# Performance work log

Hardware: AMD Instinct MI355X
Metric: run time of the kernel (lower is better)

## Reference

```python
import jax, jax.numpy as jnp
import numpy as np

# DeTok Decoder ('base'): width=768, layers=12, heads=12, head_dim=64, grid=16, seq=256
B, N, G, P = 64, 256, 16, 16
W, L, H, D = 768, 12, 12, 64
HID, TC = 2048, 16  # SwiGLU hidden = int(2/3*768*4.0); token_channels
EPS = 1e-6


def make_rope(dim=D, seq_h=G, seq_w=G, max_freq=7.0, min_freq=0.0007):
    f1 = max_freq * (max_freq / min_freq) ** np.linspace(0, -1, dim // 4)
    f1 = np.concatenate([f1, f1])                      # [dim//2]
    f2 = np.zeros((2, dim))
    f2[0, : dim // 2] = f1
    f2[1, dim // 2 :] = f1
    f2 = f2 * 2.0 * np.pi
    cx = np.linspace(0, 1, seq_h)
    cy = np.linspace(0, 1, seq_w)
    coords = np.stack(np.meshgrid(cx, cy, indexing='ij'), -1).reshape(-1, 2)  # cartesian_prod order
    ang = coords @ f2                                   # [N, dim]
    return np.concatenate([np.cos(ang), np.sin(ang)], -1).astype(np.float32)  # [N, 2*dim]


def setup_inputs() -> dict:
    key = jax.random.key(0)
    ks = jax.random.split(key, 16)
    s = 0.02
    inp = {
        'z_latents': jax.random.normal(ks[0], (B, N, TC), jnp.float32),
        'pos_emb':   jax.random.normal(ks[1], (1, N, W), jnp.float32) * (W ** -0.5),
        'W_embed':   jax.random.normal(ks[2], (TC, W), jnp.float32) * s,
        'b_embed':   jnp.zeros((W,), jnp.float32),
        'ln_pre_w':  jnp.ones((W,), jnp.float32),
        'n1_w':      jnp.ones((L, W), jnp.float32),
        'qkv_w':     jax.random.normal(ks[3], (L, W, 3 * W), jnp.float32) * s,
        'qkv_b':     jnp.zeros((L, 3 * W), jnp.float32),
        'proj_w':    jax.random.normal(ks[4], (L, W, W), jnp.float32) * s,
        'proj_b':    jnp.zeros((L, W), jnp.float32),
        'n2_w':      jnp.ones((L, W), jnp.float32),
        'w12_w':     jax.random.normal(ks[5], (L, W, 2 * HID), jnp.float32) * s,
        'w12_b':     jnp.zeros((L, 2 * HID), jnp.float32),
        'w3_w':      jax.random.normal(ks[6], (L, HID, W), jnp.float32) * s,
        'w3_b':      jnp.zeros((L, W), jnp.float32),
        'ln_post_w': jnp.ones((W,), jnp.float32),
        'conv1_w':   jax.random.normal(ks[7], (W, P * P * 3), jnp.float32) * s,  # 1x1 conv as matmul
        'conv1_b':   jnp.zeros((P * P * 3,), jnp.float32),
        'conv_out_w': jax.random.normal(ks[8], (3, 3, 3, 3), jnp.float32) * s,   # OIHW
        'conv_out_b': jnp.zeros((3,), jnp.float32),
        'rope':      jnp.asarray(make_rope()),          # [N, 2*D] buffer
    }
    return inp


def _rms(x, w):
    return x * jax.lax.rsqrt(jnp.mean(x * x, axis=-1, keepdims=True) + EPS) * w


def _rotate_half(x):
    x1, x2 = x[..., 0::2], x[..., 1::2]
    return jnp.stack((-x2, x1), axis=-1).reshape(x.shape)


def reference(z_latents, pos_emb, W_embed, b_embed, ln_pre_w, n1_w, qkv_w, qkv_b,
              proj_w, proj_b, n2_w, w12_w, w12_b, w3_w, w3_b, ln_post_w,
              conv1_w, conv1_b, conv_out_w, conv_out_b, rope):
    bsz = z_latents.shape[0]
    cos = rope[None, None, :, :D]   # [1,1,N,D]
    sin = rope[None, None, :, D:]
    scale = 1.0 / jnp.sqrt(jnp.float32(D))

    z = z_latents @ W_embed + b_embed          # [B,N,W]
    z = z + pos_emb
    z = _rms(z, ln_pre_w)

    def block(z, p):
        n1, qw, qb, pw, pb, n2, a12w, a12b, a3w, a3b = p
        h = _rms(z, n1)
        qkv = (h @ qw + qb).reshape(bsz, N, 3, H, D).transpose(2, 0, 3, 1, 4)  # [3,B,H,N,D]
        q, k, v = qkv[0], qkv[1], qkv[2]
        q = q * cos + _rotate_half(q) * sin
        k = k * cos + _rotate_half(k) * sin
        att = jax.nn.softmax(jnp.einsum('bhnd,bhmd->bhnm', q, k) * scale, axis=-1)
        o = jnp.einsum('bhnm,bhmd->bhnd', att, v).transpose(0, 2, 1, 3).reshape(bsz, N, W)
        z = z + o @ pw + pb
        h = _rms(z, n2)
        x12 = h @ a12w + a12b
        x1, x2 = x12[..., :HID], x12[..., HID:]
        z = z + (jax.nn.silu(x1) * x2) @ a3w + a3b
        return z, None

    z, _ = jax.lax.scan(block, z, (n1_w, qkv_w, qkv_b, proj_w, proj_b,
                                   n2_w, w12_w, w12_b, w3_w, w3_b))
    z = _rms(z, ln_post_w)
    # 1x1 conv (width -> P*P*3) then pixel-unshuffle: b (h w) (p1 p2 c) -> b c (h p1) (w p2)
    y = z @ conv1_w + conv1_b                   # [B,N,P*P*3]
    y = y.reshape(bsz, G, G, P, P, 3).transpose(0, 5, 1, 3, 2, 4).reshape(bsz, 3, G * P, G * P)
    out = jax.lax.conv_general_dilated(y, conv_out_w, (1, 1), 'SAME',
                                       dimension_numbers=('NCHW', 'OIHW', 'NCHW'))
    return out + conv_out_b[None, :, None, None]
```

## Files before the change

kernel.cpp:

```cpp
#include <hip/hip_runtime.h>
#include <stdint.h>

typedef unsigned short u16;
typedef __attribute__((ext_vector_type(8))) short short8;
typedef __attribute__((ext_vector_type(4))) float f32x4;

__device__ __forceinline__ float bflo(unsigned int u) {
  union { unsigned int i; float f; } x; x.i = u << 16; return x.f;
}
__device__ __forceinline__ float bfhi(unsigned int u) {
  union { unsigned int i; float f; } x; x.i = u & 0xffff0000u; return x.f;
}
__device__ __forceinline__ float bf2f(u16 u) {
  union { unsigned int i; float f; } x; x.i = ((unsigned int)u) << 16; return x.f;
}
__device__ __forceinline__ u16 f2bf(float f) {
  union { float f; unsigned int i; } x; x.f = f;
  unsigned int r = x.i + 0x7fffu + ((x.i >> 16) & 1u);
  return (u16)(r >> 16);
}

typedef __attribute__((address_space(1))) const unsigned int as1_uint;
typedef __attribute__((address_space(3))) unsigned int as3_uint;

__device__ __forceinline__ void gload_lds16(const void* g, void* l) {
  __builtin_amdgcn_global_load_lds(
      (const as1_uint*)(unsigned long long)g,
      (as3_uint*)(unsigned int)(unsigned long long)l,
      16, 0, 0);
}

__device__ __forceinline__ short8 dsr128(const void* p) {
  short8 r;
  asm volatile("ds_read_b128 %0, %1"
               : "=v"(r)
               : "v"((unsigned int)(unsigned long long)p));
  return r;
}

#define FENCE() asm volatile("" ::: "memory")
#define BAR() do { FENCE(); __builtin_amdgcn_s_barrier(); FENCE(); } while (0)
#define VMCNT(n) asm volatile("s_waitcnt vmcnt(" #n ")" ::: "memory")
#define LGKM0_SB() do { asm volatile("s_waitcnt lgkmcnt(0)"); __builtin_amdgcn_sched_barrier(0); } while (0)

__global__ __launch_bounds__(256) void transpose_conv(const float* __restrict__ in, u16* __restrict__ out,
                                                      int K, int N, int perm) {
  __shared__ float tile[32][33];
  const long l = blockIdx.z;
  int nb = blockIdx.x;
  int nbsrc = nb;
  if (perm == 2) {
    nbsrc = (nb & 1) ? 64 + (nb >> 1) : (nb >> 1);
  }
  const int nbS = nbsrc * 32;
  const int nbD = nb * 32;
  const int kb = blockIdx.y * 32;
  const float* I = in + l * (long)K * N;
  u16* O = out + l * (long)N * K;
  const int tx = threadIdx.x, ty = threadIdx.y;
#pragma unroll
  for (int i = 0; i < 32; i += 8)
    tile[ty + i][tx] = I[(long)(kb + ty + i) * N + nbS + tx];
  __syncthreads();
#pragma unroll
  for (int i = 0; i < 32; i += 8)
    O[(long)(nbD + ty + i) * K + kb + tx] = f2bf(tile[tx][ty + i]);
}

__global__ __launch_bounds__(256) void embed_kernel(const float* __restrict__ zl, const float* __restrict__ pos,
                                                    const float* __restrict__ We, const float* __restrict__ be,
                                                    const float* __restrict__ lnw, float* __restrict__ z) {
  const long row = blockIdx.x;
  const int n = (int)(row & 255);
  const int t = threadIdx.x;
  __shared__ float zc[16];
  __shared__ float wsum[4];
  if (t < 16) zc[t] = zl[row * 16 + t];
  __syncthreads();
  float v[3];
#pragma unroll
  for (int e = 0; e < 3; ++e) {
    const int col = t + e * 256;
    float s = be[col] + pos[(long)n * 768 + col];
#pragma unroll
    for (int c = 0; c < 16; ++c) s += zc[c] * We[c * 768 + col];
    v[e] = s;
  }
  float ss = v[0] * v[0] + v[1] * v[1] + v[2] * v[2];
#pragma unroll
  for (int off = 32; off > 0; off >>= 1) ss += __shfl_down(ss, off, 64);
  if ((t & 63) == 0) wsum[t >> 6] = ss;
  __syncthreads();
  const float tot = wsum[0] + wsum[1] + wsum[2] + wsum[3];
  const float rs = rsqrtf(tot * (1.f / 768.f) + 1e-6f);
#pragma unroll
  for (int e = 0; e < 3; ++e) {
    const int col = t + e * 256;
    z[row * 768 + col] = v[e] * rs * lnw[col];
  }
}

__global__ __launch_bounds__(256) void rms_wave(const float* __restrict__ z, const float* __restrict__ w,
                                                u16* __restrict__ h) {
  const int lane = threadIdx.x & 63;
  const int wv = threadIdx.x >> 6;
  float4 wl[3];
#pragma unroll
  for (int k = 0; k < 3; ++k) wl[k] = *(const float4*)(w + k * 256 + lane * 4);
  const long base = ((long)blockIdx.x * 4 + wv) * 8;
  for (int r = 0; r < 8; ++r) {
    const long row = base + r;
    const float* zr = z + row * 768;
    float4 xv[3];
    float ss = 0.f;
#pragma unroll
    for (int k = 0; k < 3; ++k) {
      xv[k] = *(const float4*)(zr + k * 256 + lane * 4);
      ss += xv[k].x * xv[k].x + xv[k].y * xv[k].y + xv[k].z * xv[k].z + xv[k].w * xv[k].w;
    }
#pragma unroll
    for (int o = 1; o < 64; o <<= 1) ss += __shfl_xor(ss, o);
    const float rs = rsqrtf(ss * (1.f / 768.f) + 1e-6f);
    u16* hr = h + row * 768;
#pragma unroll
    for (int k = 0; k < 3; ++k) {
      uint2 pk;
      pk.x = (unsigned int)f2bf(xv[k].x * rs * wl[k].x) | ((unsigned int)f2bf(xv[k].y * rs * wl[k].y) << 16);
      pk.y = (unsigned int)f2bf(xv[k].z * rs * wl[k].z) | ((unsigned int)f2bf(xv[k].w * rs * wl[k].w) << 16);
      *(uint2*)(hr + k * 256 + lane * 4) = pk;
    }
  }
}

template <int OUT_MODE>
__global__ __launch_bounds__(256, 3) void gemm128s(const u16* __restrict__ A, const u16* __restrict__ Bt,
                                                   void* __restrict__ C, const float* __restrict__ bias,
                                                   int M, int N, int K, int nbn, int super,
                                                   const float* __restrict__ rope, u16* __restrict__ q_r,
                                                   u16* __restrict__ k_s, u16* __restrict__ v_t) {
  __shared__ __align__(16) char ldsc[49152];
  const int tid = threadIdx.x;
  const int lane = tid & 63;
  const int wave = tid >> 6;
  const int i = lane & 15, g = lane >> 4;
  const int wr = wave >> 1, wc = wave & 1;
  const int xsw = (i & 7) << 4;

  const int wg = blockIdx.x, nwg = gridDim.x;
  const int w2 = (wg & 7) * (nwg >> 3) + (wg >> 3);
  int bm, bn;
  if (super == 8) {
    const int s = w2 >> 6, t = w2 & 63;
    const int scols = nbn >> 3;
    bm = ((s / scols) << 3) + (t >> 3);
    bn = ((s % scols) << 3) + (t & 7);
  } else if (super == 6) {
    const int s = w2 / 48, t = w2 % 48;
    const int scols = nbn / 6;
    bm = ((s / scols) << 3) + t / 6;
    bn = (s % scols) * 6 + t % 6;
  } else {
    bm = w2 / nbn; bn = w2 - bm * nbn;
  }
  const long m0 = (long)bm * 128, n0 = (long)bn * 128;

  const u16* Ab_ = A + m0 * K;
  const u16* Bb_ = Bt + n0 * K;
  const int srow = tid >> 3;
  const int scol = ((((tid & 7) * 16) ^ ((srow & 7) << 4)) >> 1);
  const int NT = K >> 6;

  auto stageA = [&](int kk) {
    const u16* s_ = Ab_ + (long)srow * K + kk + scol;
    char* d = ldsc + wave * 1024;
    gload_lds16(s_, d);
    gload_lds16(s_ + 32L * K, d + 4096);
    gload_lds16(s_ + 64L * K, d + 8192);
    gload_lds16(s_ + 96L * K, d + 12288);
  };
  auto stageB = [&](int kk) {
    const u16* s_ = Bb_ + (long)srow * K + kk + scol;
    char* d = ldsc + 16384 + wave * 1024;
    gload_lds16(s_, d);
    gload_lds16(s_ + 32L * K, d + 4096);
    gload_lds16(s_ + 64L * K, d + 8192);
    gload_lds16(s_ + 96L * K, d + 12288);
  };

  f32x4 acc[4][4];
#pragma unroll
  for (int mf = 0; mf < 4; ++mf)
#pragma unroll
    for (int nf = 0; nf < 4; ++nf) { f32x4 zz = {0.f, 0.f, 0.f, 0.f}; acc[mf][nf] = zz; }
  short8 af[4][2], bf[4][2];
  const char* Abuf = ldsc;
  const char* Bbuf = ldsc + 16384;

#define LOAD_A()                                                                                 \
  _Pragma("unroll") for (int r = 0; r < 4; ++r) _Pragma("unroll") for (int s2 = 0; s2 < 2; ++s2) \
      af[r][s2] = dsr128(Abuf + (wr * 64 + r * 16 + i) * 128 + ((s2 * 64 + g * 16) ^ xsw));
#define LOAD_B()                                                                                 \
  _Pragma("unroll") for (int q = 0; q < 4; ++q) _Pragma("unroll") for (int s2 = 0; s2 < 2; ++s2) \
      bf[q][s2] = dsr128(Bbuf + (wc * 64 + q * 16 + i) * 128 + ((s2 * 64 + g * 16) ^ xsw));
#define MFMA_ALL()                                                                               \
  do {                                                                                           \
    __builtin_amdgcn_s_setprio(1);                                                               \
    _Pragma("unroll") for (int r = 0; r < 4; ++r)                                                \
    _Pragma("unroll") for (int q = 0; q < 4; ++q)                                                \
    _Pragma("unroll") for (int s2 = 0; s2 < 2; ++s2)                                             \
        acc[r][q] = __builtin_amdgcn_mfma_f32_16x16x32_bf16(af[r][s2], bf[q][s2], acc[r][q],     \
                                                            0, 0, 0);                            \
    __builtin_amdgcn_s_setprio(0);                                                               \
  } while (0)

  stageA(0); stageB(0);
  VMCNT(0);
  BAR();

  for (int t2 = 0; t2 < NT; ++t2) {
    const bool pf = (t2 + 1 < NT);
    const int k1 = (t2 + 1) * 64;
    LOAD_A(); LOAD_B();
    LGKM0_SB();
    BAR();
    if (pf) { stageA(k1); stageB(k1); }
    MFMA_ALL();
    if (pf) VMCNT(0);
    BAR();
  }
#undef LOAD_A
#undef LOAD_B
#undef MFMA_ALL

  if constexpr (OUT_MODE == 3) {
    u16* U = (u16*)C;
#pragma unroll
    for (int mf = 0; mf < 4; ++mf) {
      const long rowb = m0 + wr * 64 + mf * 16 + g * 4;
#pragma unroll
      for (int nf2 = 0; nf2 < 2; ++nf2) {
        const int col = bn * 64 + wc * 32 + nf2 * 16 + i;
        const float bv1 = bias[col];
        const float bv2 = bias[2048 + col];
#pragma unroll
        for (int j = 0; j < 4; ++j) {
          const float x1 = acc[mf][nf2][j] + bv1;
          const float x2 = acc[mf][nf2 + 2][j] + bv2;
          const float uu = x1 / (1.f + __expf(-x1)) * x2;
          U[(rowb + j) * 2048 + col] = f2bf(uu);
        }
      }
    }
    return;
  }

  if constexpr (OUT_MODE == 4) {
    const int sec = (int)(n0 / 768);
    const int head = ((int)(n0 % 768) >> 6) + wc;
    if (sec == 2) {
#pragma unroll
      for (int mf = 0; mf < 4; ++mf) {
        const long rowb = m0 + wr * 64 + mf * 16 + g * 4;
        const int n = (int)(rowb & 255);
        const long b = rowb >> 8;
        const long bh = b * 12 + head;
        char* vp = (char*)v_t + bh * 32768;
#pragma unroll
        for (int nf = 0; nf < 4; ++nf) {
          const int d = nf * 16 + i;
          const float bv = bias[n0 + wc * 64 + d];
          uint2 pk;
          pk.x = (unsigned int)f2bf(acc[mf][nf][0] + bv) | ((unsigned int)f2bf(acc[mf][nf][1] + bv) << 16);
          pk.y = (unsigned int)f2bf(acc[mf][nf][2] + bv) | ((unsigned int)f2bf(acc[mf][nf][3] + bv) << 16);
          *(uint2*)(vp + d * 512 + ((2 * n) ^ ((d & 7) << 4))) = pk;
        }
      }
    } else {
#pragma unroll
      for (int mf = 0; mf < 4; ++mf) {
        const long rowb = m0 + wr * 64 + mf * 16 + g * 4;
#pragma unroll
        for (int nf = 0; nf < 4; ++nf) {
          const int d = nf * 16 + i;
          const float bv = bias[n0 + wc * 64 + d];
#pragma unroll
          for (int j = 0; j < 4; ++j) {
            const long row = rowb + j;
            const int n = (int)(row & 255);
            const long b = row >> 8;
            const long bh = b * 12 + head;
            const float x = acc[mf][nf][j] + bv;
            const float px = __shfl_xor(x, 1);
            const float cs = rope[n * 128 + d];
            const float sn = rope[n * 128 + 64 + d];
            const float outv = (d & 1) ? x * cs + px * sn : x * cs - px * sn;
            if (sec == 0) {
              q_r[bh * 16384 + (long)n * 64 + d] = f2bf(outv);
            } else {
              char* kp = (char*)k_s + bh * 32768;
              *(u16*)(kp + n * 128 + ((2 * d) ^ ((n & 7) << 4))) = f2bf(outv);
            }
          }
        }
      }
    }
    return;
  }

#pragma unroll
  for (int mf = 0; mf < 4; ++mf) {
    const long row = m0 + wr * 64 + mf * 16 + g * 4;
#pragma unroll
    for (int nf = 0; nf < 4; ++nf) {
      const long col = n0 + wc * 64 + nf * 16 + i;
      const float bv = bias ? bias[col] : 0.f;
#pragma unroll
      for (int j = 0; j < 4; ++j) {
        const float v = acc[mf][nf][j] + bv;
        if constexpr (OUT_MODE == 0) ((float*)C)[(row + j) * N + col] = v;
        else ((float*)C)[(row + j) * N + col] += v;
      }
    }
  }
}

__global__ __launch_bounds__(256) void attn_kernel(const u16* __restrict__ q_r, const u16* __restrict__ k_s,
                                                   const u16* __restrict__ v_t, u16* __restrict__ out) {
  __shared__ __align__(16) u16 Kl[16384];
  __shared__ __align__(16) u16 VTl[16384];
  __shared__ __align__(16) u16 Pl[8192];
  const int tid = threadIdx.x;
  const int lane = tid & 63;
  const int w = tid >> 6;
  const int i = lane & 15;
  const int g = lane >> 4;
  const long bh = blockIdx.x;
  const u16* kg = k_s + bh * 16384;
  const u16* vg = v_t + bh * 16384;
#pragma unroll
  for (int p = 0; p < 8; ++p) {
    gload_lds16(kg + p * 2048 + tid * 8, &Kl[p * 2048 + w * 512]);
    gload_lds16(vg + p * 2048 + tid * 8, &VTl[p * 2048 + w * 512]);
  }
  __syncthreads();

  short8 qv[4][2];
  const u16* qbase = q_r + bh * 16384;
#pragma unroll
  for (int qf = 0; qf < 4; ++qf) {
#pragma unroll
    for (int kc = 0; kc < 2; ++kc)
      qv[qf][kc] = *(const short8*)(qbase + (w * 64 + qf * 16 + i) * 64 + kc * 32 + g * 8);
  }

  f32x4 o[4][4];
#pragma unroll
  for (int df = 0; df < 4; ++df)
#pragma unroll
    for (int qf = 0; qf < 4; ++qf) { f32x4 zz = {0.f, 0.f, 0.f, 0.f}; o[df][qf] = zz; }
  float m[4], l[4];
#pragma unroll
  for (int qf = 0; qf < 4; ++qf) { m[qf] = -1e30f; l[qf] = 0.f; }

  char* pw = (char*)Pl + w * 4096;

  for (int c = 0; c < 8; ++c) {
    f32x4 st[2][4];
#pragma unroll
    for (int f = 0; f < 2; ++f)
#pragma unroll
      for (int qf = 0; qf < 4; ++qf) { f32x4 zz = {0.f, 0.f, 0.f, 0.f}; st[f][qf] = zz; }
    __builtin_amdgcn_s_setprio(1);
#pragma unroll
    for (int f = 0; f < 2; ++f) {
      const int kv = c * 32 + f * 16 + i;
#pragma unroll
      for (int kc = 0; kc < 2; ++kc) {
        short8 kf = *(const short8*)((const char*)Kl + kv * 128 + (((kc * 64 + g * 16)) ^ ((kv & 7) << 4)));
#pragma unroll
        for (int qf = 0; qf < 4; ++qf)
          st[f][qf] = __builtin_amdgcn_mfma_f32_16x16x32_bf16(kf, qv[qf][kc], st[f][qf], 0, 0, 0);
      }
    }
    __builtin_amdgcn_s_setprio(0);
#pragma unroll
    for (int qf = 0; qf < 4; ++qf) {
      float s[8];
#pragma unroll
      for (int f = 0; f < 2; ++f)
#pragma unroll
        for (int j = 0; j < 4; ++j) s[f * 4 + j] = st[f][qf][j] * 0.125f;
      float cm = fmaxf(fmaxf(fmaxf(s[0], s[1]), fmaxf(s[2], s[3])),
                       fmaxf(fmaxf(s[4], s[5]), fmaxf(s[6], s[7])));
      cm = fmaxf(cm, __shfl_xor(cm, 16));
      cm = fmaxf(cm, __shfl_xor(cm, 32));
      const bool upd = cm > m[qf] + 8.f;
      const float newm = upd ? cm : m[qf];
      const float fac = __expf(m[qf] - newm);
      float psum = 0.f;
      u16 pb[8];
#pragma unroll
      for (int t2 = 0; t2 < 8; ++t2) {
        const float p = __expf(s[t2] - newm);
        psum += p;
        pb[t2] = f2bf(p);
      }
      l[qf] = l[qf] * fac + psum;
      m[qf] = newm;
      if (__any(upd)) {
#pragma unroll
        for (int df = 0; df < 4; ++df)
#pragma unroll
          for (int j = 0; j < 4; ++j) o[df][qf][j] *= fac;
      }
      char* pbase = pw + (qf * 16 + i) * 64 + g * 8;
      uint2 w0, w1;
      w0.x = (unsigned int)pb[0] | ((unsigned int)pb[1] << 16);
      w0.y = (unsigned int)pb[2] | ((unsigned int)pb[3] << 16);
      w1.x = (unsigned int)pb[4] | ((unsigned int)pb[5] << 16);
      w1.y = (unsigned int)pb[6] | ((unsigned int)pb[7] << 16);
      *(uint2*)(pbase) = w0;
      *(uint2*)(pbase + 32) = w1;
    }
    short8 pf[4];
#pragma unroll
    for (int qf = 0; qf < 4; ++qf)
      pf[qf] = *(const short8*)(pw + (qf * 16 + i) * 64 + g * 16);
    __builtin_amdgcn_s_setprio(1);
#pragma unroll
    for (int df = 0; df < 4; ++df) {
      const int d = df * 16 + i;
      short8 vf = *(const short8*)((const char*)VTl + d * 512 + ((c * 64 + g * 16) ^ ((d & 7) << 4)));
#pragma unroll
      for (int qf = 0; qf < 4; ++qf)
        o[df][qf] = __builtin_amdgcn_mfma_f32_16x16x32_bf16(vf, pf[qf], o[df][qf], 0, 0, 0);
    }
    __builtin_amdgcn_s_setprio(0);
  }

#pragma unroll
  for (int qf = 0; qf < 4; ++qf) {
    l[qf] += __shfl_xor(l[qf], 16);
    l[qf] += __shfl_xor(l[qf], 32);
  }

  const long b = bh / 12;
  const int hh = (int)(bh % 12);
#pragma unroll
  for (int qf = 0; qf < 4; ++qf) {
    const float inv = 1.f / l[qf];
    const long q = w * 64 + qf * 16 + i;
    u16* op = out + (b * 256 + q) * 768 + hh * 64;
#pragma unroll
    for (int df = 0; df < 4; ++df) {
      const int d0 = df * 16 + g * 4;
      unsigned int a = (unsigned int)f2bf(o[df][qf][0] * inv) | ((unsigned int)f2bf(o[df][qf][1] * inv) << 16);
      unsigned int bb = (unsigned int)f2bf(o[df][qf][2] * inv) | ((unsigned int)f2bf(o[df][qf][3] * inv) << 16);
      *(unsigned int*)(op + d0) = a;
      *(unsigned int*)(op + d0 + 2) = bb;
    }
  }
}

__global__ __launch_bounds__(256) void conv_out_kernel(const float* __restrict__ y, const float* __restrict__ w,
                                                       const float* __restrict__ cb, float* __restrict__ out) {
  __shared__ float buf[18 * 258 * 3];
  __shared__ float wl[81];
  __shared__ float cbl[3];
  const int tid = threadIdx.x;
  const int gh = blockIdx.x;
  const long b = blockIdx.y;
  for (int idx = tid; idx < 18 * 258 * 3; idx += 256) buf[idx] = 0.f;
  if (tid < 81) wl[tid] = w[tid];
  if (tid < 3) cbl[tid] = cb[tid];
  __syncthreads();
  const float* yb = y + (b * 256 + gh * 16) * 768;
  for (int idx = tid; idx < 12288; idx += 256) {
    const int gw = idx / 768, col = idx - gw * 768;
    const int ph = col / 48, rem = col - ph * 48;
    const int pw = rem / 3, ii = rem - pw * 3;
    buf[((ph + 1) * 258 + gw * 16 + pw + 1) * 3 + ii] = yb[idx];
  }
  if (gh > 0) {
    const float* yh = y + (b * 256 + (gh - 1) * 16) * 768;
    for (int idx = tid; idx < 768; idx += 256) {
      const int gw = idx / 48, rem = idx - gw * 48;
      const int pw = rem / 3, ii = rem - pw * 3;
      buf[(gw * 16 + pw + 1) * 3 + ii] = yh[gw * 768 + 720 + rem];
    }
  }
  if (gh < 15) {
    const float* yh = y + (b * 256 + (gh + 1) * 16) * 768;
    for (int idx = tid; idx < 768; idx += 256) {
      const int gw = idx / 48, rem = idx - gw * 48;
      const int pw = rem / 3, ii = rem - pw * 3;
      buf[(17 * 258 + gw * 16 + pw + 1) * 3 + ii] = yh[gw * 768 + rem];
    }
  }
  __syncthreads();
  const int c = tid;
  for (int rl = 0; rl < 16; ++rl) {
    float a0 = cbl[0], a1 = cbl[1], a2 = cbl[2];
#pragma unroll
    for (int ky = 0; ky < 3; ++ky)
#pragma unroll
      for (int kx = 0; kx < 3; ++kx)
#pragma unroll
        for (int ii = 0; ii < 3; ++ii) {
          const float v = buf[((rl + ky) * 258 + c + kx) * 3 + ii];
          const int wi = ii * 9 + ky * 3 + kx;
          a0 += v * wl[wi];
          a1 += v * wl[27 + wi];
          a2 += v * wl[54 + wi];
        }
    const long r = gh * 16 + rl;
    out[((b * 3 + 0) * 256 + r) * 256 + c] = a0;
    out[((b * 3 + 1) * 256 + r) * 256 + c] = a1;
    out[((b * 3 + 2) * 256 + r) * 256 + c] = a2;
  }
}

extern "C" void kernel_launch(void* const* d_in, const int* in_sizes, int n_in,
                              void* d_out, int out_size, void* d_ws, size_t ws_size,
                              hipStream_t stream) {
  const float* z_latents = (const float*)d_in[0];
  const float* pos_emb   = (const float*)d_in[1];
  const float* W_embed   = (const float*)d_in[2];
  const float* b_embed   = (const float*)d_in[3];
  const float* ln_pre_w  = (const float*)d_in[4];
  const float* n1_w      = (const float*)d_in[5];
  const float* qkv_w     = (const float*)d_in[6];
  const float* qkv_b     = (const float*)d_in[7];
  const float* proj_w    = (const float*)d_in[8];
  const float* proj_b    = (const float*)d_in[9];
  const float* n2_w      = (const float*)d_in[10];
  const float* w12_w     = (const float*)d_in[11];
  const float* w12_b     = (const float*)d_in[12];
  const float* w3_w      = (const float*)d_in[13];
  const float* w3_b      = (const float*)d_in[14];
  const float* ln_post_w = (const float*)d_in[15];
  const float* conv1_w   = (const float*)d_in[16];
  const float* conv1_b   = (const float*)d_in[17];
  const float* conv_ow   = (const float*)d_in[18];
  const float* conv_ob   = (const float*)d_in[19];
  const float* rope      = (const float*)d_in[20];

  if (ws_size < 598867968ULL) return;
  char* p = (char*)d_ws;
  auto alloc = [&](size_t bytes) { char* r = p; p += (bytes + 255) & ~(size_t)255; return r; };
  float* z    = (float*)alloc(16384L * 768 * 4);
  u16*   h    = (u16*)alloc(16384L * 768 * 2);
  u16*   big  = (u16*)alloc(16384L * 4096 * 2);
  u16*   q_r  = (u16*)alloc(16384L * 768 * 2);
  u16*   k_s  = (u16*)alloc(16384L * 768 * 2);
  u16*   v_t  = (u16*)alloc(16384L * 768 * 2);
  u16*   ao   = (u16*)alloc(16384L * 768 * 2);
  u16*   u    = (u16*)alloc(16384L * 2048 * 2);
  float* y    = (float*)alloc(16384L * 768 * 4);
  u16* qkvT   = (u16*)alloc(12L * 2304 * 768 * 2);
  u16* projT  = (u16*)alloc(12L * 768 * 768 * 2);
  u16* w12T   = (u16*)alloc(12L * 4096 * 768 * 2);
  u16* w3T    = (u16*)alloc(12L * 768 * 2048 * 2);
  u16* c1T    = (u16*)alloc(768L * 768 * 2);
  (void)big;

  const dim3 tb(32, 8);
  transpose_conv<<<dim3(72, 24, 12), tb, 0, stream>>>(qkv_w, qkvT, 768, 2304, 0);
  transpose_conv<<<dim3(24, 24, 12), tb, 0, stream>>>(proj_w, projT, 768, 768, 0);
  transpose_conv<<<dim3(128, 24, 12), tb, 0, stream>>>(w12_w, w12T, 768, 4096, 2);
  transpose_conv<<<dim3(24, 64, 12), tb, 0, stream>>>(w3_w, w3T, 2048, 768, 0);
  transpose_conv<<<dim3(24, 24, 1), tb, 0, stream>>>(conv1_w, c1T, 768, 768, 0);

  embed_kernel<<<16384, 256, 0, stream>>>(z_latents, pos_emb, W_embed, b_embed, ln_pre_w, z);

  for (int l = 0; l < 12; ++l) {
    rms_wave<<<512, 256, 0, stream>>>(z, n1_w + l * 768, h);
    gemm128s<4><<<2304, 256, 0, stream>>>(h, qkvT + (long)l * 2304 * 768, nullptr,
                                          qkv_b + l * 2304, 16384, 2304, 768, 18, 6,
                                          rope, q_r, k_s, v_t);
    attn_kernel<<<768, 256, 0, stream>>>(q_r, k_s, v_t, ao);
    gemm128s<2><<<768, 256, 0, stream>>>(ao, projT + (long)l * 768 * 768, z,
                                         proj_b + l * 768, 16384, 768, 768, 6, 0,
                                         nullptr, nullptr, nullptr, nullptr);
    rms_wave<<<512, 256, 0, stream>>>(z, n2_w + l * 768, h);
    gemm128s<3><<<4096, 256, 0, stream>>>(h, w12T + (long)l * 4096 * 768, u,
                                          w12_b + l * 4096, 16384, 4096, 768, 32, 8,
                                          nullptr, nullptr, nullptr, nullptr);
    gemm128s<2><<<768, 256, 0, stream>>>(u, w3T + (long)l * 768 * 2048, z,
                                         w3_b + l * 768, 16384, 768, 2048, 6, 0,
                                         nullptr, nullptr, nullptr, nullptr);
  }

  rms_wave<<<512, 256, 0, stream>>>(z, ln_post_w, h);
  gemm128s<0><<<768, 256, 0, stream>>>(h, c1T, y, conv1_b, 16384, 768, 768, 6, 0,
                                       nullptr, nullptr, nullptr, nullptr);
  conv_out_kernel<<<dim3(16, 64), 256, 0, stream>>>(y, conv_ow, conv_ob, (float*)d_out);
}
```

Baseline: 4.791 ms.

## Replace 128x128 GEMM with 256x256 double-buffered 8-wave GEMM pipeline

Replaces the 128x128-tile, 4-wave GEMM with a 256x256-tile, 8-wave kernel that double-buffers A and B tiles in 128KB of LDS. It interleaves quarter-tile MFMA groups with staged global-to-LDS prefetches. Larger tiles raise arithmetic intensity and cut global traffic per FLOP, and the staged prefetch is meant to hide load latency behind MFMAs. The supertile grouping is dropped, and the small N=768 GEMMs now launch only 192 workgroups, which risks underfilling the GPU. The heavy LDS use also limits occupancy to one block per CU.

```diff
diff --git a/kernel.cpp b/kernel.cpp
--- a/kernel.cpp
+++ b/kernel.cpp
@@ -5,12 +5,6 @@
 typedef __attribute__((ext_vector_type(8))) short short8;
 typedef __attribute__((ext_vector_type(4))) float f32x4;
 
-__device__ __forceinline__ float bflo(unsigned int u) {
-  union { unsigned int i; float f; } x; x.i = u << 16; return x.f;
-}
-__device__ __forceinline__ float bfhi(unsigned int u) {
-  union { unsigned int i; float f; } x; x.i = u & 0xffff0000u; return x.f;
-}
 __device__ __forceinline__ float bf2f(u16 u) {
   union { unsigned int i; float f; } x; x.i = ((unsigned int)u) << 16; return x.f;
 }
@@ -133,36 +127,23 @@
 }
 
 template <int OUT_MODE>
-__global__ __launch_bounds__(256, 3) void gemm128s(const u16* __restrict__ A, const u16* __restrict__ Bt,
-                                                   void* __restrict__ C, const float* __restrict__ bias,
-                                                   int M, int N, int K, int nbn, int super,
-                                                   const float* __restrict__ rope, u16* __restrict__ q_r,
-                                                   u16* __restrict__ k_s, u16* __restrict__ v_t) {
-  __shared__ __align__(16) char ldsc[49152];
+__global__ __launch_bounds__(512, 2) void gemm256(const u16* __restrict__ A, const u16* __restrict__ Bt,
+                                                  void* __restrict__ C, const float* __restrict__ bias,
+                                                  int N, int K, int nbn,
+                                                  const float* __restrict__ rope, u16* __restrict__ q_r,
+                                                  u16* __restrict__ k_s, u16* __restrict__ v_t) {
+  __shared__ __align__(16) char ldsc[131072];
   const int tid = threadIdx.x;
   const int lane = tid & 63;
   const int wave = tid >> 6;
   const int i = lane & 15, g = lane >> 4;
-  const int wr = wave >> 1, wc = wave & 1;
+  const int wr = wave >> 2, wc = wave & 3;
   const int xsw = (i & 7) << 4;
 
   const int wg = blockIdx.x, nwg = gridDim.x;
   const int w2 = (wg & 7) * (nwg >> 3) + (wg >> 3);
-  int bm, bn;
-  if (super == 8) {
-    const int s = w2 >> 6, t = w2 & 63;
-    const int scols = nbn >> 3;
-    bm = ((s / scols) << 3) + (t >> 3);
-    bn = ((s % scols) << 3) + (t & 7);
-  } else if (super == 6) {
-    const int s = w2 / 48, t = w2 % 48;
-    const int scols = nbn / 6;
-    bm = ((s / scols) << 3) + t / 6;
-    bn = (s % scols) * 6 + t % 6;
-  } else {
-    bm = w2 / nbn; bn = w2 - bm * nbn;
-  }
-  const long m0 = (long)bm * 128, n0 = (long)bn * 128;
+  const int bm = w2 / nbn, bn = w2 - bm * nbn;
+  const long m0 = (long)bm * 256, n0 = (long)bn * 256;
 
   const u16* Ab_ = A + m0 * K;
   const u16* Bb_ = Bt + n0 * K;
@@ -170,76 +151,107 @@
   const int scol = ((((tid & 7) * 16) ^ ((srow & 7) << 4)) >> 1);
   const int NT = K >> 6;
 
-  auto stageA = [&](int kk) {
-    const u16* s_ = Ab_ + (long)srow * K + kk + scol;
-    char* d = ldsc + wave * 1024;
+  auto stageA = [&](int t, int h) {
+    const u16* s_ = Ab_ + (long)(h * 128 + srow) * K + t * 64 + scol;
+    char* d = ldsc + (t & 1) * 32768 + h * 16384 + wave * 1024;
     gload_lds16(s_, d);
-    gload_lds16(s_ + 32L * K, d + 4096);
     gload_lds16(s_ + 64L * K, d + 8192);
-    gload_lds16(s_ + 96L * K, d + 12288);
   };
-  auto stageB = [&](int kk) {
-    const u16* s_ = Bb_ + (long)srow * K + kk + scol;
-    char* d = ldsc + 16384 + wave * 1024;
+
+  f32x4 acc[8][4];
+#pragma unroll
+  for (int mf = 0; mf < 8; ++mf)
+#pragma unroll
+    for (int nf = 0; nf < 4; ++nf) { f32x4 zz = {0.f, 0.f, 0.f, 0.f}; acc[mf][nf] = zz; }
+  short8 af[4][2], b0f[2][2], b1f[2][2];
+
+#define LOAD_A(MH)                                                                                \
+  _Pragma("unroll") for (int r = 0; r < 4; ++r) _Pragma("unroll") for (int s2 = 0; s2 < 2; ++s2)  \
+      af[r][s2] = dsr128(Ab + (wr * 128 + (MH) * 64 + r * 16 + i) * 128 + ((s2 * 64 + g * 16) ^ xsw));
+#define LOAD_B(NH, BF)                                                                            \
+  _Pragma("unroll") for (int q = 0; q < 2; ++q) _Pragma("unroll") for (int s2 = 0; s2 < 2; ++s2)  \
+      BF[q][s2] = dsr128(Bb + (wc * 64 + (NH) * 32 + q * 16 + i) * 128 + ((s2 * 64 + g * 16) ^ xsw));
+#define MFMA_Q(MB, NB, BF)                                                                        \
+  do {                                                                                            \
+    __builtin_amdgcn_s_setprio(1);                                                                \
+    _Pragma("unroll") for (int r = 0; r < 4; ++r)                                                 \
+    _Pragma("unroll") for (int q = 0; q < 2; ++q)                                                 \
+    _Pragma("unroll") for (int s2 = 0; s2 < 2; ++s2)                                              \
+        acc[(MB) + r][(NB) + q] = __builtin_amdgcn_mfma_f32_16x16x32_bf16(                        \
+            af[r][s2], BF[q][s2], acc[(MB) + r][(NB) + q], 0, 0, 0);                              \
+    __builtin_amdgcn_s_setprio(0);                                                                \
+  } while (0)
+
+  stageA(0, 0); stageA(0, 1);
+  {
+    const u16* s_ = Bb_ + (long)srow * K + scol;
+    char* d = ldsc + 65536 + wave * 1024;
     gload_lds16(s_, d);
-    gload_lds16(s_ + 32L * K, d + 4096);
     gload_lds16(s_ + 64L * K, d + 8192);
-    gload_lds16(s_ + 96L * K, d + 12288);
-  };
-
-  f32x4 acc[4][4];
-#pragma unroll
-  for (int mf = 0; mf < 4; ++mf)
-#pragma unroll
-    for (int nf = 0; nf < 4; ++nf) { f32x4 zz = {0.f, 0.f, 0.f, 0.f}; acc[mf][nf] = zz; }
-  short8 af[4][2], bf[4][2];
-  const char* Abuf = ldsc;
-  const char* Bbuf = ldsc + 16384;
-
-#define LOAD_A()                                                                                 \
-  _Pragma("unroll") for (int r = 0; r < 4; ++r) _Pragma("unroll") for (int s2 = 0; s2 < 2; ++s2) \
-      af[r][s2] = dsr128(Abuf + (wr * 64 + r * 16 + i) * 128 + ((s2 * 64 + g * 16) ^ xsw));
-#define LOAD_B()                                                                                 \
-  _Pragma("unroll") for (int q = 0; q < 4; ++q) _Pragma("unroll") for (int s2 = 0; s2 < 2; ++s2) \
-      bf[q][s2] = dsr128(Bbuf + (wc * 64 + q * 16 + i) * 128 + ((s2 * 64 + g * 16) ^ xsw));
-#define MFMA_ALL()                                                                               \
-  do {                                                                                           \
-    __builtin_amdgcn_s_setprio(1);                                                               \
-    _Pragma("unroll") for (int r = 0; r < 4; ++r)                                                \
-    _Pragma("unroll") for (int q = 0; q < 4; ++q)                                                \
-    _Pragma("unroll") for (int s2 = 0; s2 < 2; ++s2)                                             \
-        acc[r][q] = __builtin_amdgcn_mfma_f32_16x16x32_bf16(af[r][s2], bf[q][s2], acc[r][q],     \
-                                                            0, 0, 0);                            \
-    __builtin_amdgcn_s_setprio(0);                                                               \
-  } while (0)
-
-  stageA(0); stageB(0);
-  VMCNT(0);
+    gload_lds16(s_ + 128L * K, d + 16384);
+    gload_lds16(s_ + 192L * K, d + 24576);
+  }
+  if (NT > 1) {
+    const u16* s_ = Bb_ + (long)srow * K + 64 + scol;
+    char* d = ldsc + 65536 + 32768 + wave * 1024;
+    gload_lds16(s_, d);
+    gload_lds16(s_ + 64L * K, d + 8192);
+    gload_lds16(s_ + 128L * K, d + 16384);
+    gload_lds16(s_ + 192L * K, d + 24576);
+  }
+  VMCNT(4);
   BAR();
 
-  for (int t2 = 0; t2 < NT; ++t2) {
-    const bool pf = (t2 + 1 < NT);
-    const int k1 = (t2 + 1) * 64;
-    LOAD_A(); LOAD_B();
+  for (int t = 0; t < NT; ++t) {
+    const char* Ab = ldsc + (t & 1) * 32768;
+    const char* Bb = ldsc + 65536 + (t & 1) * 32768;
+    const bool p1ok = (t + 1 < NT), p2ok = (t + 2 < NT);
+    LOAD_A(0); LOAD_B(0, b0f);
+    if (p1ok) stageA(t + 1, 0);
+    BAR();
     LGKM0_SB();
-    BAR();
-    if (pf) { stageA(k1); stageB(k1); }
-    MFMA_ALL();
-    if (pf) VMCNT(0);
+    MFMA_Q(0, 0, b0f);
+    BAR();
+    LOAD_B(1, b1f);
+    if (p1ok) stageA(t + 1, 1);
+    BAR();
+    LGKM0_SB();
+    MFMA_Q(0, 2, b1f);
+    BAR();
+    LOAD_A(1);
+    if (p2ok) {
+      const u16* s_ = Bb_ + (long)srow * K + (t + 2) * 64 + scol;
+      char* d = ldsc + 65536 + (t & 1) * 32768 + wave * 1024;
+      gload_lds16(s_, d);
+      gload_lds16(s_ + 64L * K, d + 8192);
+    }
+    BAR();
+    LGKM0_SB();
+    MFMA_Q(4, 2, b1f);
+    BAR();
+    if (p2ok) {
+      const u16* s_ = Bb_ + (long)(128 + srow) * K + (t + 2) * 64 + scol;
+      char* d = ldsc + 65536 + (t & 1) * 32768 + 16384 + wave * 1024;
+      gload_lds16(s_, d);
+      gload_lds16(s_ + 64L * K, d + 8192);
+    }
+    VMCNT(4);
+    BAR();
+    MFMA_Q(4, 0, b0f);
     BAR();
   }
 #undef LOAD_A
 #undef LOAD_B
-#undef MFMA_ALL
+#undef MFMA_Q
 
   if constexpr (OUT_MODE == 3) {
     u16* U = (u16*)C;
 #pragma unroll
-    for (int mf = 0; mf < 4; ++mf) {
-      const long rowb = m0 + wr * 64 + mf * 16 + g * 4;
+    for (int mf = 0; mf < 8; ++mf) {
+      const long rowb = m0 + wr * 128 + (mf >> 2) * 64 + (mf & 3) * 16 + g * 4;
 #pragma unroll
       for (int nf2 = 0; nf2 < 2; ++nf2) {
-        const int col = bn * 64 + wc * 32 + nf2 * 16 + i;
+        const int col = (int)(n0 >> 1) + wc * 32 + nf2 * 16 + i;
         const float bv1 = bias[col];
         const float bv2 = bias[2048 + col];
 #pragma unroll
@@ -259,15 +271,14 @@
     const int head = ((int)(n0 % 768) >> 6) + wc;
     if (sec == 2) {
 #pragma unroll
-      for (int mf = 0; mf < 4; ++mf) {
-        const long rowb = m0 + wr * 64 + mf * 16 + g * 4;
+      for (int mf = 0; mf < 8; ++mf) {
+        const long rowb = m0 + wr * 128 + (mf >> 2) * 64 + (mf & 3) * 16 + g * 4;
         const int n = (int)(rowb & 255);
         const long b = rowb >> 8;
-        const long bh = b * 12 + head;
-        char* vp = (char*)v_t + bh * 32768;
+        char* vp = (char*)v_t + (b * 12 + head) * 32768;
 #pragma unroll
         for (int nf = 0; nf < 4; ++nf) {
-          const int d = nf * 16 + i;
+          const int d = (nf >> 1) * 32 + (nf & 1) * 16 + i;
           const float bv = bias[n0 + wc * 64 + d];
           uint2 pk;
           pk.x = (unsigned int)f2bf(acc[mf][nf][0] + bv) | ((unsigned int)f2bf(acc[mf][nf][1] + bv) << 16);
@@ -277,11 +288,11 @@
       }
     } else {
 #pragma unroll
-      for (int mf = 0; mf < 4; ++mf) {
-        const long rowb = m0 + wr * 64 + mf * 16 + g * 4;
+      for (int mf = 0; mf < 8; ++mf) {
+        const long rowb = m0 + wr * 128 + (mf >> 2) * 64 + (mf & 3) * 16 + g * 4;
 #pragma unroll
         for (int nf = 0; nf < 4; ++nf) {
-          const int d = nf * 16 + i;
+          const int d = (nf >> 1) * 32 + (nf & 1) * 16 + i;
           const float bv = bias[n0 + wc * 64 + d];
 #pragma unroll
           for (int j = 0; j < 4; ++j) {
@@ -308,11 +319,11 @@
   }
 
 #pragma unroll
-  for (int mf = 0; mf < 4; ++mf) {
-    const long row = m0 + wr * 64 + mf * 16 + g * 4;
+  for (int mf = 0; mf < 8; ++mf) {
+    const long row = m0 + wr * 128 + (mf >> 2) * 64 + (mf & 3) * 16 + g * 4;
 #pragma unroll
     for (int nf = 0; nf < 4; ++nf) {
-      const long col = n0 + wc * 64 + nf * 16 + i;
+      const long col = n0 + wc * 64 + (nf >> 1) * 32 + (nf & 1) * 16 + i;
       const float bv = bias ? bias[col] : 0.f;
 #pragma unroll
       for (int j = 0; j < 4; ++j) {
@@ -575,24 +586,24 @@
 
   for (int l = 0; l < 12; ++l) {
     rms_wave<<<512, 256, 0, stream>>>(z, n1_w + l * 768, h);
-    gemm128s<4><<<2304, 256, 0, stream>>>(h, qkvT + (long)l * 2304 * 768, nullptr,
-                                          qkv_b + l * 2304, 16384, 2304, 768, 18, 6,
-                                          rope, q_r, k_s, v_t);
+    gemm256<4><<<576, 512, 0, stream>>>(h, qkvT + (long)l * 2304 * 768, nullptr,
+                                        qkv_b + l * 2304, 2304, 768, 9,
+                                        rope, q_r, k_s, v_t);
     attn_kernel<<<768, 256, 0, stream>>>(q_r, k_s, v_t, ao);
-    gemm128s<2><<<768, 256, 0, stream>>>(ao, projT + (long)l * 768 * 768, z,
-                                         proj_b + l * 768, 16384, 768, 768, 6, 0,
+    gemm256<2><<<192, 512, 0, stream>>>(ao, projT + (long)l * 768 * 768, z,
+                                        proj_b + l * 768, 768, 768, 3,
+                                        nullptr, nullptr, nullptr, nullptr);
+    rms_wave<<<512, 256, 0, stream>>>(z, n2_w + l * 768, h);
+    gemm256<3><<<1024, 512, 0, stream>>>(h, w12T + (long)l * 4096 * 768, u,
+                                         w12_b + l * 4096, 4096, 768, 16,
                                          nullptr, nullptr, nullptr, nullptr);
-    rms_wave<<<512, 256, 0, stream>>>(z, n2_w + l * 768, h);
-    gemm128s<3><<<4096, 256, 0, stream>>>(h, w12T + (long)l * 4096 * 768, u,
-                                          w12_b + l * 4096, 16384, 4096, 768, 32, 8,
-                                          nullptr, nullptr, nullptr, nullptr);
-    gemm128s<2><<<768, 256, 0, stream>>>(u, w3T + (long)l * 768 * 2048, z,
-                                         w3_b + l * 768, 16384, 768, 2048, 6, 0,
-                                         nullptr, nullptr, nullptr, nullptr);
+    gemm256<2><<<192, 512, 0, stream>>>(u, w3T + (long)l * 768 * 2048, z,
+                                        w3_b + l * 768, 768, 2048, 3,
+                                        nullptr, nullptr, nullptr, nullptr);
   }
 
   rms_wave<<<512, 256, 0, stream>>>(z, ln_post_w, h);
-  gemm128s<0><<<768, 256, 0, stream>>>(h, c1T, y, conv1_b, 16384, 768, 768, 6, 0,
-                                       nullptr, nullptr, nullptr, nullptr);
+  gemm256<0><<<192, 512, 0, stream>>>(h, c1T, y, conv1_b, 768, 768, 3,
+                                      nullptr, nullptr, nullptr, nullptr);
   conv_out_kernel<<<dim3(16, 64), 256, 0, stream>>>(y, conv_ow, conv_ob, (float*)d_out);
 }
```

Result: slower. 5.713 ms (+19.2%).

## Add 256x256-tile, 8-wave GEMM for QKV and SwiGLU up-projection

Applied to the files above, without the earlier changes.

Adds a new GEMM kernel with 256x256 output tiles, 512 threads, double-buffered LDS staging through global_load_lds, and a ping-pong schedule of fragment loads and MFMA quarters. It is used for the QKV projection (with RoPE and the q/k/v layout epilogue) and for the w12 SwiGLU projection, replacing the 128x128 kernel there. Larger tiles raise arithmetic intensity and reuse per LDS byte, at the cost of 128 KB of LDS per block, higher register pressure, and fewer workgroups (576 and 1024) that may fill the CUs less evenly.

```diff
diff --git a/kernel.cpp b/kernel.cpp
--- a/kernel.cpp
+++ b/kernel.cpp
@@ -5,12 +5,6 @@
 typedef __attribute__((ext_vector_type(8))) short short8;
 typedef __attribute__((ext_vector_type(4))) float f32x4;
 
-__device__ __forceinline__ float bflo(unsigned int u) {
-  union { unsigned int i; float f; } x; x.i = u << 16; return x.f;
-}
-__device__ __forceinline__ float bfhi(unsigned int u) {
-  union { unsigned int i; float f; } x; x.i = u & 0xffff0000u; return x.f;
-}
 __device__ __forceinline__ float bf2f(u16 u) {
   union { unsigned int i; float f; } x; x.i = ((unsigned int)u) << 16; return x.f;
 }
@@ -313,6 +307,198 @@
 #pragma unroll
     for (int nf = 0; nf < 4; ++nf) {
       const long col = n0 + wc * 64 + nf * 16 + i;
+      const float bv = bias ? bias[col] : 0.f;
+#pragma unroll
+      for (int j = 0; j < 4; ++j) {
+        const float v = acc[mf][nf][j] + bv;
+        if constexpr (OUT_MODE == 0) ((float*)C)[(row + j) * N + col] = v;
+        else ((float*)C)[(row + j) * N + col] += v;
+      }
+    }
+  }
+}
+
+template <int OUT_MODE>
+__global__ __launch_bounds__(512, 2) void gemm256(const u16* __restrict__ A, const u16* __restrict__ Bt,
+                                                  void* __restrict__ C, const float* __restrict__ bias,
+                                                  int N, int K, int nbn,
+                                                  const float* __restrict__ rope, u16* __restrict__ q_r,
+                                                  u16* __restrict__ k_s, u16* __restrict__ v_t) {
+  __shared__ __align__(16) char ldsc[131072];
+  const int tid = threadIdx.x;
+  const int lane = tid & 63;
+  const int wave = tid >> 6;
+  const int i = lane & 15, g = lane >> 4;
+  const int wr = wave >> 2, wc = wave & 3;
+  const int xsw = (i & 7) << 4;
+
+  const int wg = blockIdx.x, nwg = gridDim.x;
+  const int w2 = (wg & 7) * (nwg >> 3) + (wg >> 3);
+  const int bm = w2 / nbn, bn = w2 - bm * nbn;
+  const long m0 = (long)bm * 256, n0 = (long)bn * 256;
+
+  const u16* Ab_ = A + m0 * K;
+  const u16* Bb_ = Bt + n0 * K;
+  const int srow = tid >> 3;
+  const int scol = ((((tid & 7) * 16) ^ ((srow & 7) << 4)) >> 1);
+  const int NT = K >> 6;
+
+  auto stageA = [&](int t, int h) {
+    const u16* s_ = Ab_ + (long)(h * 128 + srow) * K + t * 64 + scol;
+    char* d = ldsc + (t & 1) * 32768 + h * 16384 + wave * 1024;
+    gload_lds16(s_, d);
+    gload_lds16(s_ + 64L * K, d + 8192);
+  };
+  auto stageB = [&](int t, int h) {
+    const u16* s_ = Bb_ + (long)(h * 128 + srow) * K + t * 64 + scol;
+    char* d = ldsc + 65536 + (t & 1) * 32768 + h * 16384 + wave * 1024;
+    gload_lds16(s_, d);
+    gload_lds16(s_ + 64L * K, d + 8192);
+  };
+
+  f32x4 acc[8][4];
+#pragma unroll
+  for (int mf = 0; mf < 8; ++mf)
+#pragma unroll
+    for (int nf = 0; nf < 4; ++nf) { f32x4 zz = {0.f, 0.f, 0.f, 0.f}; acc[mf][nf] = zz; }
+  short8 af[4][2], b0f[2][2], b1f[2][2];
+
+#define LOAD_A(MH)                                                                                \
+  _Pragma("unroll") for (int r = 0; r < 4; ++r) _Pragma("unroll") for (int s2 = 0; s2 < 2; ++s2)  \
+      af[r][s2] = dsr128(Ab + (wr * 128 + (MH) * 64 + r * 16 + i) * 128 + ((s2 * 64 + g * 16) ^ xsw));
+#define LOAD_B(NH, BF)                                                                            \
+  _Pragma("unroll") for (int q = 0; q < 2; ++q) _Pragma("unroll") for (int s2 = 0; s2 < 2; ++s2)  \
+      BF[q][s2] = dsr128(Bb + (wc * 64 + (NH) * 32 + q * 16 + i) * 128 + ((s2 * 64 + g * 16) ^ xsw));
+#define MFMA_Q(MB, NB, BF)                                                                        \
+  do {                                                                                            \
+    __builtin_amdgcn_s_setprio(1);                                                                \
+    _Pragma("unroll") for (int r = 0; r < 4; ++r)                                                 \
+    _Pragma("unroll") for (int q = 0; q < 2; ++q)                                                 \
+    _Pragma("unroll") for (int s2 = 0; s2 < 2; ++s2)                                              \
+        acc[(MB) + r][(NB) + q] = __builtin_amdgcn_mfma_f32_16x16x32_bf16(                        \
+            af[r][s2], BF[q][s2], acc[(MB) + r][(NB) + q], 0, 0, 0);                              \
+    __builtin_amdgcn_s_setprio(0);                                                                \
+  } while (0)
+
+  stageA(0, 0); stageA(0, 1); stageB(0, 0); stageB(0, 1);
+  if (NT > 1) { stageA(1, 0); stageA(1, 1); stageB(1, 0); stageB(1, 1); }
+  VMCNT(8);
+  BAR();
+
+  for (int t = 0; t < NT; ++t) {
+    const char* Ab = ldsc + (t & 1) * 32768;
+    const char* Bb = ldsc + 65536 + (t & 1) * 32768;
+    const bool p2ok = (t + 2 < NT);
+    LOAD_A(0); LOAD_B(0, b0f);
+    BAR();
+    LGKM0_SB();
+    MFMA_Q(0, 0, b0f);
+    BAR();
+    LOAD_B(1, b1f);
+    BAR();
+    LGKM0_SB();
+    MFMA_Q(0, 2, b1f);
+    BAR();
+    LOAD_A(1);
+    if (p2ok) { stageB(t + 2, 0); stageB(t + 2, 1); }
+    BAR();
+    LGKM0_SB();
+    MFMA_Q(4, 2, b1f);
+    BAR();
+    if (p2ok) {
+      stageA(t + 2, 0); stageA(t + 2, 1);
+      VMCNT(8);
+    } else {
+      VMCNT(0);
+    }
+    BAR();
+    MFMA_Q(4, 0, b0f);
+    BAR();
+  }
+#undef LOAD_A
+#undef LOAD_B
+#undef MFMA_Q
+
+  if constexpr (OUT_MODE == 3) {
+    u16* U = (u16*)C;
+#pragma unroll
+    for (int mf = 0; mf < 8; ++mf) {
+      const long rowb = m0 + wr * 128 + (mf >> 2) * 64 + (mf & 3) * 16 + g * 4;
+#pragma unroll
+      for (int nf2 = 0; nf2 < 2; ++nf2) {
+        const int col = (int)(n0 >> 1) + wc * 32 + nf2 * 16 + i;
+        const float bv1 = bias[col];
+        const float bv2 = bias[2048 + col];
+#pragma unroll
+        for (int j = 0; j < 4; ++j) {
+          const float x1 = acc[mf][nf2][j] + bv1;
+          const float x2 = acc[mf][nf2 + 2][j] + bv2;
+          const float uu = x1 / (1.f + __expf(-x1)) * x2;
+          U[(rowb + j) * 2048 + col] = f2bf(uu);
+        }
+      }
+    }
+    return;
+  }
+
+  if constexpr (OUT_MODE == 4) {
+    const int sec = (int)(n0 / 768);
+    const int head = ((int)(n0 % 768) >> 6) + wc;
+    if (sec == 2) {
+#pragma unroll
+      for (int mf = 0; mf < 8; ++mf) {
+        const long rowb = m0 + wr * 128 + (mf >> 2) * 64 + (mf & 3) * 16 + g * 4;
+        const int n = (int)(rowb & 255);
+        const long b = rowb >> 8;
+        char* vp = (char*)v_t + (b * 12 + head) * 32768;
+#pragma unroll
+        for (int nf = 0; nf < 4; ++nf) {
+          const int d = (nf >> 1) * 32 + (nf & 1) * 16 + i;
+          const float bv = bias[n0 + wc * 64 + d];
+          uint2 pk;
+          pk.x = (unsigned int)f2bf(acc[mf][nf][0] + bv) | ((unsigned int)f2bf(acc[mf][nf][1] + bv) << 16);
+          pk.y = (unsigned int)f2bf(acc[mf][nf][2] + bv) | ((unsigned int)f2bf(acc[mf][nf][3] + bv) << 16);
+          *(uint2*)(vp + d * 512 + ((2 * n) ^ ((d & 7) << 4))) = pk;
+        }
+      }
+    } else {
+#pragma unroll
+      for (int mf = 0; mf < 8; ++mf) {
+        const long rowb = m0 + wr * 128 + (mf >> 2) * 64 + (mf & 3) * 16 + g * 4;
+#pragma unroll
+        for (int nf = 0; nf < 4; ++nf) {
+          const int d = (nf >> 1) * 32 + (nf & 1) * 16 + i;
+          const float bv = bias[n0 + wc * 64 + d];
+#pragma unroll
+          for (int j = 0; j < 4; ++j) {
+            const long row = rowb + j;
+            const int n = (int)(row & 255);
+            const long b = row >> 8;
+            const long bh = b * 12 + head;
+            const float x = acc[mf][nf][j] + bv;
+            const float px = __shfl_xor(x, 1);
+            const float cs = rope[n * 128 + d];
+            const float sn = rope[n * 128 + 64 + d];
+            const float outv = (d & 1) ? x * cs + px * sn : x * cs - px * sn;
+            if (sec == 0) {
+              q_r[bh * 16384 + (long)n * 64 + d] = f2bf(outv);
+            } else {
+              char* kp = (char*)k_s + bh * 32768;
+              *(u16*)(kp + n * 128 + ((2 * d) ^ ((n & 7) << 4))) = f2bf(outv);
+            }
+          }
+        }
+      }
+    }
+    return;
+  }
+
+#pragma unroll
+  for (int mf = 0; mf < 8; ++mf) {
+    const long row = m0 + wr * 128 + (mf >> 2) * 64 + (mf & 3) * 16 + g * 4;
+#pragma unroll
+    for (int nf = 0; nf < 4; ++nf) {
+      const long col = n0 + wc * 64 + (nf >> 1) * 32 + (nf & 1) * 16 + i;
       const float bv = bias ? bias[col] : 0.f;
 #pragma unroll
       for (int j = 0; j < 4; ++j) {
@@ -575,17 +761,17 @@
 
   for (int l = 0; l < 12; ++l) {
     rms_wave<<<512, 256, 0, stream>>>(z, n1_w + l * 768, h);
-    gemm128s<4><<<2304, 256, 0, stream>>>(h, qkvT + (long)l * 2304 * 768, nullptr,
-                                          qkv_b + l * 2304, 16384, 2304, 768, 18, 6,
-                                          rope, q_r, k_s, v_t);
+    gemm256<4><<<576, 512, 0, stream>>>(h, qkvT + (long)l * 2304 * 768, nullptr,
+                                        qkv_b + l * 2304, 2304, 768, 9,
+                                        rope, q_r, k_s, v_t);
     attn_kernel<<<768, 256, 0, stream>>>(q_r, k_s, v_t, ao);
     gemm128s<2><<<768, 256, 0, stream>>>(ao, projT + (long)l * 768 * 768, z,
                                          proj_b + l * 768, 16384, 768, 768, 6, 0,
                                          nullptr, nullptr, nullptr, nullptr);
     rms_wave<<<512, 256, 0, stream>>>(z, n2_w + l * 768, h);
-    gemm128s<3><<<4096, 256, 0, stream>>>(h, w12T + (long)l * 4096 * 768, u,
-                                          w12_b + l * 4096, 16384, 4096, 768, 32, 8,
-                                          nullptr, nullptr, nullptr, nullptr);
+    gemm256<3><<<1024, 512, 0, stream>>>(h, w12T + (long)l * 4096 * 768, u,
+                                         w12_b + l * 4096, 4096, 768, 16,
+                                         nullptr, nullptr, nullptr, nullptr);
     gemm128s<2><<<768, 256, 0, stream>>>(u, w3T + (long)l * 768 * 2048, z,
                                          w3_b + l * 768, 16384, 768, 2048, 6, 0,
                                          nullptr, nullptr, nullptr, nullptr);
```

After: 5.332 ms. 11.3% more time.
